# Optimization experiments

Measured on AMD Instinct MI355X. Metric: run time of the kernel, lower is better.

The kernel has to match this reference:

```python
import jax, jax.numpy as jnp
import numpy as np

B, S, D, H = 4, 2048, 1024, 16
DK = D // H


def setup_inputs() -> dict:
    key = jax.random.key(0)
    ks = jax.random.split(key, 12)
    s = 1.0 / np.sqrt(D)
    inp = {
        "query": jax.random.normal(ks[0], (B, S, D), jnp.float32),
        "key": jax.random.normal(ks[1], (B, S, D), jnp.float32),
        "value": jax.random.normal(ks[2], (B, S, D), jnp.float32),
        "mask": jax.random.randint(ks[3], (B, S, S), 0, 2, jnp.int32),
        "Wq": jax.random.uniform(ks[4], (D, D), jnp.float32, -s, s),
        "bq": jax.random.uniform(ks[5], (D,), jnp.float32, -s, s),
        "Wk": jax.random.uniform(ks[6], (D, D), jnp.float32, -s, s),
        "bk": jax.random.uniform(ks[7], (D,), jnp.float32, -s, s),
        "Wv": jax.random.uniform(ks[8], (D, D), jnp.float32, -s, s),
        "bv": jax.random.uniform(ks[9], (D,), jnp.float32, -s, s),
        "Wo": jax.random.uniform(ks[10], (D, D), jnp.float32, -s, s),
        "bo": jax.random.uniform(ks[11], (D,), jnp.float32, -s, s),
    }
    return inp


def reference(query, key, value, mask, Wq, bq, Wk, bk, Wv, bv, Wo, bo):
    # Linear projections (torch Linear: x @ W.T + b), split into heads: [B,H,S,DK]
    def proj(x, W, b):
        y = x @ W.T + b
        return y.reshape(B, S, H, DK).transpose(0, 2, 1, 3)

    q = proj(query, Wq, bq)
    k = proj(key, Wk, bk)
    v = proj(value, Wv, bv)

    # scores: [B,H,S,S]
    scores = jnp.einsum("bhqd,bhkd->bhqk", q, k) / jnp.sqrt(jnp.float32(DK))
    m = mask[:, None, :, :]  # broadcast over heads
    scores = jnp.where(m == 0, jnp.float32(-1e9), scores)
    attn = jax.nn.softmax(scores, axis=-1)
    out = jnp.einsum("bhqk,bhkd->bhqd", attn, v)
    out = out.transpose(0, 2, 1, 3).reshape(B, S, D)
    return out @ Wo.T + bo
```

## Files before the change

kernel.cpp:

```cpp
#include <hip/hip_runtime.h>

#define B_  4
#define S_  2048
#define D_  1024
#define H_  16
#define DK_ 64

typedef __attribute__((ext_vector_type(8))) __bf16 bf16x8;
typedef __attribute__((ext_vector_type(4))) float  f32x4;

#define AS1 __attribute__((address_space(1)))
#define AS3 __attribute__((address_space(3)))

__device__ __forceinline__ void gl2lds16(const void* g, void* l) {
    __builtin_amdgcn_global_load_lds((const AS1 unsigned int*)g,
                                     (AS3 unsigned int*)l, 16, 0, 0);
}

__device__ __forceinline__ unsigned short f2bf(float f) {
    union { float f; unsigned u; } v; v.f = f;
    return (unsigned short)((v.u + 0x7FFFu + ((v.u >> 16) & 1u)) >> 16);
}

__device__ __forceinline__ unsigned pk_bf16(float f0, float f1) {
    union { float f; unsigned u; } a, b; a.f = f0; b.f = f1;
    return __builtin_amdgcn_perm(b.u + 0x8000u, a.u + 0x8000u, 0x07060302u);
}

__device__ __forceinline__ void cast8(const float* __restrict__ x,
                                      unsigned short* __restrict__ y, int i) {
    float4 a = ((const float4*)x)[2 * i];
    float4 b = ((const float4*)x)[2 * i + 1];
    uint4 w;
    w.x = pk_bf16(a.x, a.y);
    w.y = pk_bf16(a.z, a.w);
    w.z = pk_bf16(b.x, b.y);
    w.w = pk_bf16(b.z, b.w);
    ((uint4*)y)[i] = w;
}

__global__ __launch_bounds__(256) void cast_act(
    const float* __restrict__ a, const float* __restrict__ b,
    const float* __restrict__ c, unsigned short* __restrict__ ya,
    unsigned short* __restrict__ yb, unsigned short* __restrict__ yc)
{
    const int sel = blockIdx.y;
    const float* x = (sel == 0) ? a : (sel == 1) ? b : c;
    unsigned short* y = (sel == 0) ? ya : (sel == 1) ? yb : yc;
    cast8(x, y, blockIdx.x * 256 + threadIdx.x);
}

__global__ __launch_bounds__(256) void cast_w(
    const float* __restrict__ a, const float* __restrict__ b,
    const float* __restrict__ c, const float* __restrict__ d,
    unsigned short* __restrict__ ya, unsigned short* __restrict__ yb,
    unsigned short* __restrict__ yc, unsigned short* __restrict__ yd)
{
    const int sel = blockIdx.y;
    const float* x = (sel == 0) ? a : (sel == 1) ? b : (sel == 2) ? c : d;
    unsigned short* y = (sel == 0) ? ya : (sel == 1) ? yb : (sel == 2) ? yc : yd;
    cast8(x, y, blockIdx.x * 256 + threadIdx.x);
}

__global__ __launch_bounds__(256, 3) void gemm_qkv(
    const unsigned short* __restrict__ Xq, const unsigned short* __restrict__ Xk,
    const unsigned short* __restrict__ Xv, const unsigned short* __restrict__ Wqkv,
    const float* __restrict__ bq, const float* __restrict__ bk,
    const float* __restrict__ bv, unsigned short* __restrict__ Qw,
    unsigned short* __restrict__ Kw, unsigned short* __restrict__ Vt,
    float qscale)
{
    __shared__ unsigned short As[128 * 64];
    __shared__ unsigned short Bs[128 * 64];

    const int tid  = threadIdx.x;
    const int lane = tid & 63, wave = tid >> 6;
    const int l16  = lane & 15, quad = lane >> 4;
    const int wm = wave & 1, wn = wave >> 1;
    const int n0 = blockIdx.x * 128, m0 = blockIdx.y * 128;
    const int xr = l16 & 7;

    const int sel = blockIdx.x >> 3;
    const unsigned short* X = (sel == 0) ? Xq : (sel == 1) ? Xk : Xv;

    const int row8 = lane >> 3;
    const int sc   = ((lane & 7) ^ row8) * 8;

    f32x4 acc[4][4] = {};

    for (int k0 = 0; k0 < D_; k0 += 64) {
        __syncthreads();
        #pragma unroll
        for (int j = 0; j < 4; ++j) {
            const int ca = wave * 4 + j;
            const int r  = ca * 8 + row8;
            gl2lds16(X    + (size_t)(m0 + r) * D_ + k0 + sc, &As[ca * 512 + (lane & 63) * 8]);
            gl2lds16(Wqkv + (size_t)(n0 + r) * D_ + k0 + sc, &Bs[ca * 512 + (lane & 63) * 8]);
        }
        __syncthreads();

        #pragma unroll
        for (int s = 0; s < 2; ++s) {
            bf16x8 a[4], bb[4];
            #pragma unroll
            for (int i = 0; i < 4; ++i)
                a[i] = *(const bf16x8*)&As[(wm * 64 + i * 16 + l16) * 64 + (((s * 4 + quad) ^ xr)) * 8];
            #pragma unroll
            for (int j = 0; j < 4; ++j)
                bb[j] = *(const bf16x8*)&Bs[(wn * 64 + j * 16 + l16) * 64 + (((s * 4 + quad) ^ xr)) * 8];
            #pragma unroll
            for (int i = 0; i < 4; ++i)
                #pragma unroll
                for (int j = 0; j < 4; ++j)
                    acc[i][j] = __builtin_amdgcn_mfma_f32_16x16x32_bf16(a[i], bb[j], acc[i][j], 0, 0, 0);
        }
    }

    const int ncol = (blockIdx.x & 7) * 128 + wn * 64;
    const float scale = (sel == 0) ? qscale : 1.0f;
    const float* bias = (sel == 0) ? bq : (sel == 1) ? bk : bv;

    if (sel == 2) {
        const int bb_ = m0 >> 11;
        #pragma unroll
        for (int j = 0; j < 4; ++j) {
            const int dk = ncol + j * 16 + l16;
            const float bvv = bias[dk];
            #pragma unroll
            for (int i = 0; i < 4; ++i) {
                const int sb = (m0 & (S_ - 1)) + wm * 64 + i * 16 + quad * 4;
                uint2 w;
                w.x = pk_bf16(acc[i][j][0] + bvv, acc[i][j][1] + bvv);
                w.y = pk_bf16(acc[i][j][2] + bvv, acc[i][j][3] + bvv);
                *(uint2*)(Vt + (size_t)(bb_ * D_ + dk) * S_ + sb) = w;
            }
        }
    } else {
        unsigned short* Outp = sel ? Kw : Qw;
        #pragma unroll
        for (int j = 0; j < 4; ++j) {
            const int n = ncol + j * 16 + l16;
            const float bvv = bias[n];
            #pragma unroll
            for (int i = 0; i < 4; ++i) {
                #pragma unroll
                for (int r = 0; r < 4; ++r) {
                    const int m = m0 + wm * 64 + i * 16 + quad * 4 + r;
                    Outp[(size_t)m * D_ + n] = f2bf((acc[i][j][r] + bvv) * scale);
                }
            }
        }
    }
}

__global__ __launch_bounds__(256, 3) void gemm_out(
    const unsigned short* __restrict__ X, const unsigned short* __restrict__ W,
    const float* __restrict__ bias, float* __restrict__ Out)
{
    __shared__ unsigned short As[128 * 64];
    __shared__ unsigned short Bs[128 * 64];

    const int tid  = threadIdx.x;
    const int lane = tid & 63, wave = tid >> 6;
    const int l16  = lane & 15, quad = lane >> 4;
    const int wm = wave & 1, wn = wave >> 1;
    const int n0 = blockIdx.x * 128, m0 = blockIdx.y * 128;
    const int xr = l16 & 7;

    const int row8 = lane >> 3;
    const int sc   = ((lane & 7) ^ row8) * 8;

    f32x4 acc[4][4] = {};

    for (int k0 = 0; k0 < D_; k0 += 64) {
        __syncthreads();
        #pragma unroll
        for (int j = 0; j < 4; ++j) {
            const int ca = wave * 4 + j;
            const int r  = ca * 8 + row8;
            gl2lds16(X + (size_t)(m0 + r) * D_ + k0 + sc, &As[ca * 512 + (lane & 63) * 8]);
            gl2lds16(W + (size_t)(n0 + r) * D_ + k0 + sc, &Bs[ca * 512 + (lane & 63) * 8]);
        }
        __syncthreads();

        #pragma unroll
        for (int s = 0; s < 2; ++s) {
            bf16x8 a[4], bb[4];
            #pragma unroll
            for (int i = 0; i < 4; ++i)
                a[i] = *(const bf16x8*)&As[(wm * 64 + i * 16 + l16) * 64 + (((s * 4 + quad) ^ xr)) * 8];
            #pragma unroll
            for (int j = 0; j < 4; ++j)
                bb[j] = *(const bf16x8*)&Bs[(wn * 64 + j * 16 + l16) * 64 + (((s * 4 + quad) ^ xr)) * 8];
            #pragma unroll
            for (int i = 0; i < 4; ++i)
                #pragma unroll
                for (int j = 0; j < 4; ++j)
                    acc[i][j] = __builtin_amdgcn_mfma_f32_16x16x32_bf16(a[i], bb[j], acc[i][j], 0, 0, 0);
        }
    }

    #pragma unroll
    for (int j = 0; j < 4; ++j) {
        const int n = n0 + wn * 64 + j * 16 + l16;
        const float bv = bias[n];
        #pragma unroll
        for (int i = 0; i < 4; ++i) {
            #pragma unroll
            for (int r = 0; r < 4; ++r) {
                const int m = m0 + wm * 64 + i * 16 + quad * 4 + r;
                Out[(size_t)m * D_ + n] = acc[i][j][r] + bv;
            }
        }
    }
}

__global__ __launch_bounds__(256) void pack_mask(
    const int* __restrict__ mask, unsigned long long* __restrict__ pm)
{
    const int gid  = blockIdx.x * 256 + threadIdx.x;
    const int w    = gid >> 6;
    const int lane = threadIdx.x & 63;
    const int mv = mask[(size_t)w * 64 + lane];
    const unsigned long long bal = __ballot(mv != 0);
    if (lane == 0) pm[w] = bal;
}

__global__ __launch_bounds__(256, 4) void attn_kernel(
    const unsigned short* __restrict__ Q,
    const unsigned short* __restrict__ Kg,
    const unsigned short* __restrict__ Vt,
    const unsigned long long* __restrict__ pm,
    unsigned short* __restrict__ O)
{
    __shared__ unsigned short Ks[64 * 64];
    __shared__ unsigned short Vs[2][64 * 64];
    __shared__ unsigned short Ps[128 * 64];

    const int tid  = threadIdx.x;
    const int lane = tid & 63, wave = tid >> 6;
    const int l16  = lane & 15, quad = lane >> 4;

    const int n  = blockIdx.y * 16 + blockIdx.x;
    const int ns = (n & 7) * 128 + (n >> 3);
    const int b  = ns >> 8;
    const int h  = (ns >> 4) & 15;
    const int q0 = (ns & 15) * 128;
    const int xq = l16 & 7;

    union { uint4 u; bf16x8 v; } ones_u;
    ones_u.u = make_uint4(0x3F803F80u, 0x3F803F80u, 0x3F803F80u, 0x3F803F80u);
    const bf16x8 vb_ones = ones_u.v;

    bf16x8 qa[2][2];
    #pragma unroll
    for (int qf = 0; qf < 2; ++qf) {
        const unsigned short* qp =
            Q + (size_t)(b * S_ + q0 + wave * 32 + qf * 16 + l16) * D_ + h * DK_ + quad * 8;
        qa[qf][0] = *(const bf16x8*)qp;
        qa[qf][1] = *(const bf16x8*)(qp + 32);
    }

    const unsigned short* Kbase = Kg + (size_t)(b * S_) * D_ + h * DK_;
    const unsigned short* Vbase = Vt + (size_t)(b * D_ + h * DK_) * S_;

    auto stageK = [&](int kt2) {
        const int k0 = kt2 * 64;
        #pragma unroll
        for (int j = 0; j < 2; ++j) {
            const int c = j * 256 + tid;
            const int row = c >> 3;
            const int cl = (c & 7) ^ (row & 7);
            gl2lds16(Kbase + (size_t)(k0 + row) * D_ + cl * 8, &Ks[c * 8]);
        }
    };
    auto stageV = [&](int bi2, int kt2) {
        const int k0 = kt2 * 64;
        #pragma unroll
        for (int j = 0; j < 2; ++j) {
            const int c = j * 256 + tid;
            const int row = c >> 3;
            const int cl = (c & 7) ^ (row & 7);
            gl2lds16(Vbase + (size_t)row * S_ + k0 + cl * 8, &Vs[bi2][c * 8]);
        }
    };

    const unsigned long long* pmq0 =
        pm + (size_t)(b * S_ + q0 + wave * 32 + l16) * (S_ / 64);
    const unsigned long long* pmq1 = pmq0 + (size_t)16 * (S_ / 64);

    f32x4 oacc[2][5] = {};

    stageK(0);
    stageV(0, 0);
    __syncthreads();

    int bi = 0;
    for (int kt = 0; kt < S_ / 64; ++kt) {
        const bool more = (kt + 1 < S_ / 64);
        const unsigned long long wq0 = pmq0[kt];
        const unsigned long long wq1 = pmq1[kt];
        if (more) stageV(bi ^ 1, kt + 1);

        #pragma unroll
        for (int half = 0; half < 2; ++half) {
            f32x4 sct[2][2] = {};
            __builtin_amdgcn_s_setprio(1);
            #pragma unroll
            for (int s = 0; s < 2; ++s) {
                const int cs = ((s * 4 + quad) ^ xq) * 8;
                #pragma unroll
                for (int mbh = 0; mbh < 2; ++mbh) {
                    bf16x8 ka = *(const bf16x8*)&Ks[((half * 2 + mbh) * 16 + l16) * 64 + cs];
                    sct[mbh][0] = __builtin_amdgcn_mfma_f32_16x16x32_bf16(ka, qa[0][s], sct[mbh][0], 0, 0, 0);
                    sct[mbh][1] = __builtin_amdgcn_mfma_f32_16x16x32_bf16(ka, qa[1][s], sct[mbh][1], 0, 0, 0);
                }
            }
            __builtin_amdgcn_s_setprio(0);

            #pragma unroll
            for (int qf = 0; qf < 2; ++qf) {
                const unsigned long long wq = qf ? wq1 : wq0;
                #pragma unroll
                for (int mbh = 0; mbh < 2; ++mbh) {
                    const int mb = half * 2 + mbh;
                    const unsigned nib = (unsigned)(wq >> (mb * 16 + quad * 4)) & 0xFu;
                    float e[4];
                    #pragma unroll
                    for (int r = 0; r < 4; ++r) {
                        float x = __builtin_amdgcn_exp2f(sct[mbh][qf][r]);
                        e[r] = ((nib >> r) & 1u) ? x : 0.f;
                    }
                    uint2 w;
                    w.x = pk_bf16(e[0], e[1]);
                    w.y = pk_bf16(e[2], e[3]);
                    *(uint2*)&Ps[(wave * 32 + qf * 16 + l16) * 64 +
                                 ((mb * 16 + quad * 4) ^ (xq * 8))] = w;
                }
            }
        }

        __syncthreads();
        if (more) stageK(kt + 1);

        __builtin_amdgcn_s_setprio(1);
        #pragma unroll
        for (int s = 0; s < 2; ++s) {
            const int cs = ((s * 4 + quad) ^ xq) * 8;
            bf16x8 pa0 = *(const bf16x8*)&Ps[(wave * 32 + l16) * 64 +
                                             ((s * 32 + quad * 8) ^ (xq * 8))];
            bf16x8 pa1 = *(const bf16x8*)&Ps[(wave * 32 + 16 + l16) * 64 +
                                             ((s * 32 + quad * 8) ^ (xq * 8))];
            #pragma unroll
            for (int db = 0; db < 4; ++db) {
                bf16x8 vb = *(const bf16x8*)&Vs[bi][(db * 16 + l16) * 64 + cs];
                oacc[0][db] = __builtin_amdgcn_mfma_f32_16x16x32_bf16(pa0, vb, oacc[0][db], 0, 0, 0);
                oacc[1][db] = __builtin_amdgcn_mfma_f32_16x16x32_bf16(pa1, vb, oacc[1][db], 0, 0, 0);
            }
            oacc[0][4] = __builtin_amdgcn_mfma_f32_16x16x32_bf16(pa0, vb_ones, oacc[0][4], 0, 0, 0);
            oacc[1][4] = __builtin_amdgcn_mfma_f32_16x16x32_bf16(pa1, vb_ones, oacc[1][4], 0, 0, 0);
        }
        __builtin_amdgcn_s_setprio(0);

        __syncthreads();
        bi ^= 1;
    }

    #pragma unroll
    for (int qf = 0; qf < 2; ++qf) {
        #pragma unroll
        for (int r = 0; r < 4; ++r) {
            const float linv = 1.0f / oacc[qf][4][r];
            const int qg = q0 + wave * 32 + qf * 16 + quad * 4 + r;
            #pragma unroll
            for (int db = 0; db < 4; ++db) {
                O[(size_t)(b * S_ + qg) * D_ + h * DK_ + db * 16 + l16] =
                    f2bf(oacc[qf][db][r] * linv);
            }
        }
    }
}

extern "C" void kernel_launch(void* const* d_in, const int* in_sizes, int n_in,
                              void* d_out, int out_size, void* d_ws, size_t ws_size,
                              hipStream_t stream)
{
    const float* q   = (const float*)d_in[0];
    const float* k   = (const float*)d_in[1];
    const float* v   = (const float*)d_in[2];
    const int* mask  = (const int*)d_in[3];
    const float* Wq  = (const float*)d_in[4];
    const float* bq  = (const float*)d_in[5];
    const float* Wk  = (const float*)d_in[6];
    const float* bk  = (const float*)d_in[7];
    const float* Wv  = (const float*)d_in[8];
    const float* bv  = (const float*)d_in[9];
    const float* Wo  = (const float*)d_in[10];
    const float* bo  = (const float*)d_in[11];

    const size_t MN = (size_t)B_ * S_ * D_;
    const size_t WN = (size_t)D_ * D_;
    unsigned short* qb  = (unsigned short*)d_ws;
    unsigned short* kb  = qb + MN;
    unsigned short* vb  = kb + MN;
    unsigned short* Qw  = vb + MN;
    unsigned short* Kw  = Qw + MN;
    unsigned short* Vt  = Kw + MN;
    unsigned short* wqb = Vt + MN;
    unsigned short* wkb = wqb + WN;
    unsigned short* wvb = wkb + WN;
    unsigned short* wob = wvb + WN;
    unsigned short* Ow  = qb;
    unsigned long long* pm = (unsigned long long*)d_out;

    dim3 blk(256);
    const int actBlocks = (int)(MN / 8 / 256);
    const int wBlocks   = (int)(WN / 8 / 256);

    pack_mask<<<(B_ * S_ * S_) / 256, blk, 0, stream>>>(mask, pm);

    cast_act<<<dim3(actBlocks, 3), blk, 0, stream>>>(q, k, v, qb, kb, vb);
    cast_w<<<dim3(wBlocks, 4), blk, 0, stream>>>(Wq, Wk, Wv, Wo, wqb, wkb, wvb, wob);

    const float qscale = 1.44269504088896341f * 0.125f;

    gemm_qkv<<<dim3(3 * D_ / 128, (B_ * S_) / 128), blk, 0, stream>>>(
        qb, kb, vb, wqb, bq, bk, bv, Qw, Kw, Vt, qscale);

    attn_kernel<<<dim3(S_ / 128, B_ * H_), blk, 0, stream>>>(Qw, Kw, Vt, pm, Ow);

    gemm_out<<<dim3(D_ / 128, (B_ * S_) / 128), blk, 0, stream>>>(
        Ow, wob, bo, (float*)d_out);
}
```

Measured before the change: 419.5 us.

## Keep softmax probabilities in registers and feed PV MFMA directly, double-buffer K

Removes the LDS round trip for the probability matrix P. The S-tile accumulator layout from the QK MFMA is reused directly as the A operand of 16x16x16 bf16 MFMAs for the PV product, with V reads remapped to match. K is now double-buffered alongside V, which removes one barrier per iteration and lets K prefetch overlap compute. It also switches to the hardware packed bf16 convert instruction. The cost is twice as many smaller MFMAs for PV and extra LDS for the second K buffer.

After: 420.9 us. About the same (+0.3%).

```diff
diff --git a/kernel.cpp b/kernel.cpp
--- a/kernel.cpp
+++ b/kernel.cpp
@@ -8,6 +8,7 @@
 
 typedef __attribute__((ext_vector_type(8))) __bf16 bf16x8;
 typedef __attribute__((ext_vector_type(4))) float  f32x4;
+typedef __attribute__((ext_vector_type(4))) short  short4v;
 
 #define AS1 __attribute__((address_space(1)))
 #define AS3 __attribute__((address_space(3)))
@@ -25,6 +26,12 @@
 __device__ __forceinline__ unsigned pk_bf16(float f0, float f1) {
     union { float f; unsigned u; } a, b; a.f = f0; b.f = f1;
     return __builtin_amdgcn_perm(b.u + 0x8000u, a.u + 0x8000u, 0x07060302u);
+}
+
+__device__ __forceinline__ unsigned cvt_pk_bf16(float lo, float hi) {
+    unsigned r;
+    asm("v_cvt_pk_bf16_f32 %0, %1, %2" : "=v"(r) : "v"(lo), "v"(hi));
+    return r;
 }
 
 __device__ __forceinline__ void cast8(const float* __restrict__ x,
@@ -233,9 +240,8 @@
     const unsigned long long* __restrict__ pm,
     unsigned short* __restrict__ O)
 {
-    __shared__ unsigned short Ks[64 * 64];
+    __shared__ unsigned short Ks[2][64 * 64];
     __shared__ unsigned short Vs[2][64 * 64];
-    __shared__ unsigned short Ps[128 * 64];
 
     const int tid  = threadIdx.x;
     const int lane = tid & 63, wave = tid >> 6;
@@ -248,9 +254,9 @@
     const int q0 = (ns & 15) * 128;
     const int xq = l16 & 7;
 
-    union { uint4 u; bf16x8 v; } ones_u;
-    ones_u.u = make_uint4(0x3F803F80u, 0x3F803F80u, 0x3F803F80u, 0x3F803F80u);
-    const bf16x8 vb_ones = ones_u.v;
+    union { uint2 u; short4v v; } ones_u;
+    ones_u.u = make_uint2(0x3F803F80u, 0x3F803F80u);
+    const short4v vb_ones = ones_u.v;
 
     bf16x8 qa[2][2];
     #pragma unroll
@@ -264,14 +270,14 @@
     const unsigned short* Kbase = Kg + (size_t)(b * S_) * D_ + h * DK_;
     const unsigned short* Vbase = Vt + (size_t)(b * D_ + h * DK_) * S_;
 
-    auto stageK = [&](int kt2) {
+    auto stageK = [&](int bi2, int kt2) {
         const int k0 = kt2 * 64;
         #pragma unroll
         for (int j = 0; j < 2; ++j) {
             const int c = j * 256 + tid;
             const int row = c >> 3;
             const int cl = (c & 7) ^ (row & 7);
-            gl2lds16(Kbase + (size_t)(k0 + row) * D_ + cl * 8, &Ks[c * 8]);
+            gl2lds16(Kbase + (size_t)(k0 + row) * D_ + cl * 8, &Ks[bi2][c * 8]);
         }
     };
     auto stageV = [&](int bi2, int kt2) {
@@ -285,13 +291,18 @@
         }
     };
 
+    int vidx[4];
+    #pragma unroll
+    for (int mb = 0; mb < 4; ++mb)
+        vidx[mb] = l16 * 64 + (((mb * 2 + (quad >> 1)) ^ xq) * 8) + (quad & 1) * 4;
+
     const unsigned long long* pmq0 =
         pm + (size_t)(b * S_ + q0 + wave * 32 + l16) * (S_ / 64);
     const unsigned long long* pmq1 = pmq0 + (size_t)16 * (S_ / 64);
 
     f32x4 oacc[2][5] = {};
 
-    stageK(0);
+    stageK(0, 0);
     stageV(0, 0);
     __syncthreads();
 
@@ -300,65 +311,59 @@
         const bool more = (kt + 1 < S_ / 64);
         const unsigned long long wq0 = pmq0[kt];
         const unsigned long long wq1 = pmq1[kt];
-        if (more) stageV(bi ^ 1, kt + 1);
-
-        #pragma unroll
-        for (int half = 0; half < 2; ++half) {
-            f32x4 sct[2][2] = {};
-            __builtin_amdgcn_s_setprio(1);
-            #pragma unroll
-            for (int s = 0; s < 2; ++s) {
-                const int cs = ((s * 4 + quad) ^ xq) * 8;
-                #pragma unroll
-                for (int mbh = 0; mbh < 2; ++mbh) {
-                    bf16x8 ka = *(const bf16x8*)&Ks[((half * 2 + mbh) * 16 + l16) * 64 + cs];
-                    sct[mbh][0] = __builtin_amdgcn_mfma_f32_16x16x32_bf16(ka, qa[0][s], sct[mbh][0], 0, 0, 0);
-                    sct[mbh][1] = __builtin_amdgcn_mfma_f32_16x16x32_bf16(ka, qa[1][s], sct[mbh][1], 0, 0, 0);
-                }
-            }
-            __builtin_amdgcn_s_setprio(0);
-
-            #pragma unroll
-            for (int qf = 0; qf < 2; ++qf) {
-                const unsigned long long wq = qf ? wq1 : wq0;
-                #pragma unroll
-                for (int mbh = 0; mbh < 2; ++mbh) {
-                    const int mb = half * 2 + mbh;
-                    const unsigned nib = (unsigned)(wq >> (mb * 16 + quad * 4)) & 0xFu;
-                    float e[4];
-                    #pragma unroll
-                    for (int r = 0; r < 4; ++r) {
-                        float x = __builtin_amdgcn_exp2f(sct[mbh][qf][r]);
-                        e[r] = ((nib >> r) & 1u) ? x : 0.f;
-                    }
-                    uint2 w;
-                    w.x = pk_bf16(e[0], e[1]);
-                    w.y = pk_bf16(e[2], e[3]);
-                    *(uint2*)&Ps[(wave * 32 + qf * 16 + l16) * 64 +
-                                 ((mb * 16 + quad * 4) ^ (xq * 8))] = w;
-                }
-            }
-        }
-
-        __syncthreads();
-        if (more) stageK(kt + 1);
-
+        if (more) {
+            stageK(bi ^ 1, kt + 1);
+            stageV(bi ^ 1, kt + 1);
+        }
+
+        f32x4 sct[4][2] = {};
         __builtin_amdgcn_s_setprio(1);
         #pragma unroll
         for (int s = 0; s < 2; ++s) {
             const int cs = ((s * 4 + quad) ^ xq) * 8;
-            bf16x8 pa0 = *(const bf16x8*)&Ps[(wave * 32 + l16) * 64 +
-                                             ((s * 32 + quad * 8) ^ (xq * 8))];
-            bf16x8 pa1 = *(const bf16x8*)&Ps[(wave * 32 + 16 + l16) * 64 +
-                                             ((s * 32 + quad * 8) ^ (xq * 8))];
+            #pragma unroll
+            for (int mb = 0; mb < 4; ++mb) {
+                bf16x8 ka = *(const bf16x8*)&Ks[bi][(mb * 16 + l16) * 64 + cs];
+                sct[mb][0] = __builtin_amdgcn_mfma_f32_16x16x32_bf16(ka, qa[0][s], sct[mb][0], 0, 0, 0);
+                sct[mb][1] = __builtin_amdgcn_mfma_f32_16x16x32_bf16(ka, qa[1][s], sct[mb][1], 0, 0, 0);
+            }
+        }
+        __builtin_amdgcn_s_setprio(0);
+
+        short4v a4[2][4];
+        #pragma unroll
+        for (int qf = 0; qf < 2; ++qf) {
+            const unsigned long long wq = qf ? wq1 : wq0;
+            #pragma unroll
+            for (int mb = 0; mb < 4; ++mb) {
+                const unsigned nib = (unsigned)(wq >> (mb * 16 + quad * 4)) & 0xFu;
+                float e[4];
+                #pragma unroll
+                for (int r = 0; r < 4; ++r) {
+                    float x = __builtin_amdgcn_exp2f(sct[mb][qf][r]);
+                    e[r] = ((nib >> r) & 1u) ? x : 0.f;
+                }
+                union { uint2 u; short4v v; } pw;
+                pw.u.x = cvt_pk_bf16(e[0], e[1]);
+                pw.u.y = cvt_pk_bf16(e[2], e[3]);
+                a4[qf][mb] = pw.v;
+            }
+        }
+
+        __builtin_amdgcn_s_setprio(1);
+        #pragma unroll
+        for (int mb = 0; mb < 4; ++mb) {
+            short4v vb[4];
+            #pragma unroll
+            for (int db = 0; db < 4; ++db)
+                vb[db] = *(const short4v*)&Vs[bi][vidx[mb] + db * 1024];
             #pragma unroll
             for (int db = 0; db < 4; ++db) {
-                bf16x8 vb = *(const bf16x8*)&Vs[bi][(db * 16 + l16) * 64 + cs];
-                oacc[0][db] = __builtin_amdgcn_mfma_f32_16x16x32_bf16(pa0, vb, oacc[0][db], 0, 0, 0);
-                oacc[1][db] = __builtin_amdgcn_mfma_f32_16x16x32_bf16(pa1, vb, oacc[1][db], 0, 0, 0);
-            }
-            oacc[0][4] = __builtin_amdgcn_mfma_f32_16x16x32_bf16(pa0, vb_ones, oacc[0][4], 0, 0, 0);
-            oacc[1][4] = __builtin_amdgcn_mfma_f32_16x16x32_bf16(pa1, vb_ones, oacc[1][4], 0, 0, 0);
+                oacc[0][db] = __builtin_amdgcn_mfma_f32_16x16x16bf16_1k(a4[0][mb], vb[db], oacc[0][db], 0, 0, 0);
+                oacc[1][db] = __builtin_amdgcn_mfma_f32_16x16x16bf16_1k(a4[1][mb], vb[db], oacc[1][db], 0, 0, 0);
+            }
+            oacc[0][4] = __builtin_amdgcn_mfma_f32_16x16x16bf16_1k(a4[0][mb], vb_ones, oacc[0][4], 0, 0, 0);
+            oacc[1][4] = __builtin_amdgcn_mfma_f32_16x16x16bf16_1k(a4[1][mb], vb_ones, oacc[1][4], 0, 0, 0);
         }
         __builtin_amdgcn_s_setprio(0);
 
```
